# Optimization experiments

Hardware: AMD Instinct MI355X
Metric: run time of the kernel (lower is better)

The kernel has to match this reference:

```python
import jax, jax.numpy as jnp
import numpy as np

EPS = 1e-7  # K.epsilon()

_LC = np.zeros((3, 3, 3), np.float32)  # Levi-Civita for 1x1->1
_LC[0, 1, 2] = _LC[1, 2, 0] = _LC[2, 0, 1] = 1.0
_LC[0, 2, 1] = _LC[2, 1, 0] = _LC[1, 0, 2] = -1.0


def _ssp(x):
    # shifted softplus: log(0.5*exp(x)+0.5)
    return jnp.log(0.5 * jnp.exp(x) + 0.5)


def _radial(image, w1, b1, w2, b2):
    # Sequential([Dense(32), Dense(feat)]) -- linear Dense layers (no activation)
    return (image @ w1 + b1) @ w2 + b2  # (m, a, b, feat)


def setup_inputs() -> dict:
    key = jax.random.key(0)
    ks = jax.random.split(key, 16)
    M, A, RBF, F, SI, H = 4, 256, 64, 32, 32, 32
    inp = {}
    inp["image"] = jax.random.uniform(ks[0], (M, A, A, RBF), dtype=jnp.float32)
    inp["vectors"] = jax.random.normal(ks[1], (M, A, A, 3), dtype=jnp.float32)
    inp["feat0"] = jax.random.normal(ks[2], (M, A, F, 1), dtype=jnp.float32)
    inp["feat1"] = jax.random.normal(ks[3], (M, A, F, 3), dtype=jnp.float32)
    i = 4
    for rin in (0, 1):
        for fro in (0, 1):
            tag = f"{rin}{fro}"
            inp[f"w1_{tag}"] = jax.random.normal(ks[i], (RBF, H)) / np.sqrt(RBF).astype(np.float32)
            inp[f"b1_{tag}"] = jnp.zeros((H,), jnp.float32)
            i += 1
            inp[f"w2_{tag}"] = jax.random.normal(ks[i], (H, F)) / np.sqrt(np.float32(H))
            inp[f"b2_{tag}"] = jnp.zeros((F,), jnp.float32)
            i += 1
    inp["w_si0"] = jax.random.normal(ks[i], (SI, 2 * F)) / np.sqrt(np.float32(2 * F)); i += 1
    inp["w_si1"] = jax.random.normal(ks[i], (SI, 3 * F)) / np.sqrt(np.float32(3 * F)); i += 1
    inp["b_act0"] = jnp.zeros((SI,), jnp.float32)
    inp["b_act1"] = jnp.zeros((SI,), jnp.float32)
    return inp


def reference(image, vectors, feat0, feat1,
              w1_00, b1_00, w2_00, b2_00,
              w1_01, b1_01, w2_01, b2_01,
              w1_10, b1_10, w2_10, b2_10,
              w1_11, b1_11, w2_11, b2_11,
              w_si0, w_si1, b_act0, b_act1):
    # mask where |r_ab| < eps (self-pairs / padding)
    mask = (jnp.sqrt(jnp.sum(vectors * vectors, axis=-1)) < EPS)[..., None]  # (m,a,b,1)

    def filt0(w1, b1, w2, b2):
        return _radial(image, w1, b1, w2, b2)  # (m,a,b,F), implicit rep index of size 1

    def filt1(w1, b1, w2, b2):
        r = jnp.where(mask, 0.0, _radial(image, w1, b1, w2, b2))  # masked radial
        return vectors[:, :, :, None, :] * r[..., None]  # (m,a,b,F,3)

    f0_in0 = filt0(w1_00, b1_00, w2_00, b2_00)
    f1_in0 = filt1(w1_01, b1_01, w2_01, b2_01)
    f0_in1 = filt0(w1_10, b1_10, w2_10, b2_10)
    f1_in1 = filt1(w1_11, b1_11, w2_11, b2_11)

    # point convolution (sum over neighbor atoms b)
    out_0x0_0 = jnp.einsum('mabf,mbfj->mafj', f0_in0, feat0)   # (m,a,F,1)
    out_0x1_1 = jnp.einsum('mabfi,mbfj->mafi', f1_in0, feat0)  # (m,a,F,3)
    out_1x0_1 = jnp.einsum('mabf,mbfj->mafj', f0_in1, feat1)   # (m,a,F,3)
    cg0 = jnp.eye(3, dtype=image.dtype)[None]                  # (1,3,3): 1x1->0
    out_1x1_0 = jnp.einsum('ijk,mabfj,mbfk->mafi', cg0, f1_in1, feat1)  # (m,a,F,1)
    lc = jnp.asarray(_LC, image.dtype)                         # 1x1->1
    out_1x1_1 = jnp.einsum('ijk,mabfj,mbfk->mafi', lc, f1_in1, feat1)   # (m,a,F,3)

    # concat along channel dim per output RO
    cat0 = jnp.concatenate([out_0x0_0, out_1x1_0], axis=2)  # (m,a,2F,1)
    cat1 = jnp.concatenate([out_0x1_1, out_1x0_1, out_1x1_1], axis=2)  # (m,a,3F,3)

    # self-interaction: einsum('mafi,gf->maig') then transpose -> (m,a,g,i)
    si0 = jnp.einsum('mafi,gf->magi', cat0, w_si0)  # (m,a,SI,1)
    si1 = jnp.einsum('mafi,gf->magi', cat1, w_si1)  # (m,a,SI,3)

    # equivariant activation
    o0 = _ssp(si0 + b_act0[None, None, :, None])
    n1 = jnp.sqrt(jnp.maximum(jnp.sum(si1 * si1, axis=-1), EPS))  # norm_with_epsilon
    a1 = _ssp(n1 + b_act1)
    o1 = si1 * (a1 / n1)[..., None]
    return (o0, o1)
```

## Files before the change

### kernel.cpp

```cpp
#include <hip/hip_runtime.h>
#include <math.h>

#define M_ 4
#define A_ 256
#define RBF_ 64
#define F_ 32
#define H_ 32
#define SI_ 32
#define TF_ 128

typedef __attribute__((ext_vector_type(8))) short bf16x8;
typedef __attribute__((ext_vector_type(4))) float f32x4;
typedef __attribute__((ext_vector_type(3))) float f32x3;

__device__ __forceinline__ unsigned short f2bf(float f) {
  union { float f; unsigned u; } v; v.f = f;
  unsigned r = v.u + 0x7FFFu + ((v.u >> 16) & 1u);
  return (unsigned short)(r >> 16);
}

__device__ __forceinline__ unsigned pack2bf(float lo, float hi) {
  union { float f; unsigned u; } a, b; a.f = lo; b.f = hi;
  return __builtin_amdgcn_perm(b.u + 0x8000u, a.u + 0x8000u, 0x07060302u);
}

__device__ __forceinline__ float sspf(float x) {
  return fmaxf(x, 0.f) + log1pf(expf(-fabsf(x))) - 0.6931471805599453f;
}

__global__ __launch_bounds__(256) void combine_weights(
    const float* __restrict__ w1_00, const float* __restrict__ b1_00,
    const float* __restrict__ w2_00, const float* __restrict__ b2_00,
    const float* __restrict__ w1_01, const float* __restrict__ b1_01,
    const float* __restrict__ w2_01, const float* __restrict__ b2_01,
    const float* __restrict__ w1_10, const float* __restrict__ b1_10,
    const float* __restrict__ w2_10, const float* __restrict__ b2_10,
    const float* __restrict__ w1_11, const float* __restrict__ b1_11,
    const float* __restrict__ w2_11, const float* __restrict__ b2_11,
    unsigned short* __restrict__ wsT, float* __restrict__ bcw)
{
  const float* w1s[4] = {w1_00, w1_01, w1_10, w1_11};
  const float* b1s[4] = {b1_00, b1_01, b1_10, b1_11};
  const float* w2s[4] = {w2_00, w2_01, w2_10, w2_11};
  const float* b2s[4] = {b2_00, b2_01, b2_10, b2_11};
  int tid = blockIdx.x * 256 + threadIdx.x;
  int k   = tid >> 7;
  int tf  = tid & 127;
  int tag = tf >> 5, f = tf & 31;
  const float* w1 = w1s[tag];
  const float* w2 = w2s[tag];
  float s = 0.f;
  for (int h = 0; h < H_; ++h) s += w1[k * H_ + h] * w2[h * F_ + f];
  wsT[tf * 64 + k] = f2bf(s);
  if (tid < TF_) {
    const float* b1 = b1s[tag];
    const float* b2 = b2s[tag];
    float sb = b2[f];
    for (int h = 0; h < H_; ++h) sb += b1[h] * w2[h * F_ + f];
    bcw[tf] = sb;
  }
}

__global__ __launch_bounds__(512, 4) void conv_main(
    const float* __restrict__ image, const float* __restrict__ vectors,
    const float* __restrict__ feat0, const float* __restrict__ feat1,
    const unsigned short* __restrict__ wsT, const float* __restrict__ bcw,
    const float* __restrict__ w_si0, const float* __restrict__ w_si1,
    const float* __restrict__ b_act0, const float* __restrict__ b_act1,
    float* __restrict__ out)
{
  __shared__ __align__(16) char smem[39936];
  unsigned short* sA  = (unsigned short*)smem;
  float*          sV  = (float*)(smem + 36864);
  float*          cat = (float*)smem;

  const int t    = threadIdx.x;
  const int ma   = blockIdx.x;
  const int m    = ma >> 8;
  const int l    = t & 63;
  const int n    = l & 15;
  const int quad = l >> 4;
  const int wu    = __builtin_amdgcn_readfirstlane(t >> 6);
  const int which = wu & 1;
  const int tag   = wu >> 1;
  const int ct    = tag * 2 + which;
  const int f     = which * 16 + n;

  const unsigned short* wr = wsT + (ct * 16 + n) * 64 + quad * 8;
  const bf16x8 w0 = *(const bf16x8*)(wr);
  const bf16x8 w1 = *(const bf16x8*)(wr + 32);
  const float  bc = bcw[ct * 16 + n];

  const float* imgMA = image + (size_t)ma * A_ * RBF_;
  #pragma unroll
  for (int i = 0; i < 4; ++i) {
    int g = t + 512 * i;
    int r = g >> 3, c8 = g & 7;
    const float* src = imgMA + r * RBF_ + c8 * 8;
    float4 v0 = *(const float4*)(src);
    float4 v1 = *(const float4*)(src + 4);
    uint4 pk;
    pk.x = pack2bf(v0.x, v0.y);
    pk.y = pack2bf(v0.z, v0.w);
    pk.z = pack2bf(v1.x, v1.y);
    pk.w = pack2bf(v1.z, v1.w);
    *(uint4*)&sA[r * 72 + c8 * 8] = pk;
  }
  #pragma unroll
  for (int i = 0; i < 2; ++i) {
    int s = t + 512 * i;
    if (s < 768) sV[s] = vectors[(size_t)ma * (A_ * 3) + s];
  }

  const float* p0 = feat0 + (size_t)(m * A_) * F_ + f;
  const float* p1 = feat1 + ((size_t)(m * A_) * F_ + f) * 3;

  float gx[2][4], gy[2][4], gz[2][4];
  float pA = 0.f, pB0 = 0.f, pB1 = 0.f, pB2 = 0.f;

#define PF(BUF, BT) { \
    const int b0 = (BT) * 16 + quad * 4; \
    if (tag <= 1) { \
      _Pragma("unroll") \
      for (int r = 0; r < 4; ++r) gx[BUF][r] = p0[(b0 + r) * F_]; \
    } else { \
      _Pragma("unroll") \
      for (int r = 0; r < 4; ++r) { \
        f32x3 v = *(const f32x3*)&p1[(size_t)(b0 + r) * (F_ * 3)]; \
        gx[BUF][r] = v[0]; gy[BUF][r] = v[1]; gz[BUF][r] = v[2]; \
      } \
    } }

#define BODY(BT, BUF) { \
    const int brow = (BT) * 16; \
    const int lb   = brow + quad * 4; \
    const bf16x8 a0 = *(const bf16x8*)&sA[(brow + n) * 72 + quad * 8]; \
    const bf16x8 a1 = *(const bf16x8*)&sA[(brow + n) * 72 + 32 + quad * 8]; \
    f32x4 acc = {bc, bc, bc, bc}; \
    acc = __builtin_amdgcn_mfma_f32_16x16x32_bf16(a0, w0, acc, 0, 0, 0); \
    acc = __builtin_amdgcn_mfma_f32_16x16x32_bf16(a1, w1, acc, 0, 0, 0); \
    if (tag == 0) {             \
      _Pragma("unroll") \
      for (int r = 0; r < 4; ++r) pA += acc[r] * gx[BUF][r]; \
    } else if (tag == 1) {      \
      _Pragma("unroll") \
      for (int r = 0; r < 4; ++r) { \
        const float s  = acc[r] * gx[BUF][r]; \
        pB0 += sV[(lb + r) * 3 + 0] * s; \
        pB1 += sV[(lb + r) * 3 + 1] * s; \
        pB2 += sV[(lb + r) * 3 + 2] * s; \
      } \
    } else if (tag == 2) {      \
      _Pragma("unroll") \
      for (int r = 0; r < 4; ++r) { \
        const float Rr = acc[r]; \
        pB0 += Rr * gx[BUF][r]; pB1 += Rr * gy[BUF][r]; pB2 += Rr * gz[BUF][r]; \
      } \
    } else {                    \
      _Pragma("unroll") \
      for (int r = 0; r < 4; ++r) { \
        const float Rr = acc[r]; \
        const float ax = gx[BUF][r], ay = gy[BUF][r], az = gz[BUF][r]; \
        const float vx = sV[(lb + r) * 3 + 0]; \
        const float vy = sV[(lb + r) * 3 + 1]; \
        const float vz = sV[(lb + r) * 3 + 2]; \
        pA  += Rr * (vx * ax + vy * ay + vz * az); \
        pB0 += Rr * (vy * az - vz * ay); \
        pB1 += Rr * (vz * ax - vx * az); \
        pB2 += Rr * (vx * ay - vy * ax); \
      } \
    } }

  PF(0, 0)
  __syncthreads();

  #pragma unroll 1
  for (int bth = 0; bth < 8; ++bth) {
    const int bt0 = bth * 2;
    PF(1, bt0 + 1)
    BODY(bt0, 0)
    if (bth < 7) PF(0, bt0 + 2)
    BODY(bt0 + 1, 1)
  }

#define QRED(x) { x += __shfl_xor(x, 16); x += __shfl_xor(x, 32); }
  QRED(pA) QRED(pB0) QRED(pB1) QRED(pB2)

  __syncthreads();
  if (quad == 0) {
    if (tag == 0) {
      cat[f] = pA;
    } else if (tag == 1) {
      cat[64 + f * 3 + 0] = pB0;
      cat[64 + f * 3 + 1] = pB1;
      cat[64 + f * 3 + 2] = pB2;
    } else if (tag == 2) {
      cat[160 + f * 3 + 0] = pB0;
      cat[160 + f * 3 + 1] = pB1;
      cat[160 + f * 3 + 2] = pB2;
    } else {
      cat[32 + f] = pA;
      cat[256 + f * 3 + 0] = pB0;
      cat[256 + f * 3 + 1] = pB1;
      cat[256 + f * 3 + 2] = pB2;
    }
  }
  __syncthreads();

  const int outBase = ma * SI_;
  if (t < 32) {
    const float* wsr = w_si0 + t * 64;
    float s = 0.f;
    #pragma unroll 8
    for (int ff = 0; ff < 64; ++ff) s += cat[ff] * wsr[ff];
    s += b_act0[t];
    out[outBase + t] = sspf(s);
  } else if (t < 64) {
    int g = t - 32;
    const float* wsr = w_si1 + g * 96;
    float s0 = 0.f, s1 = 0.f, s2 = 0.f;
    #pragma unroll 8
    for (int ff = 0; ff < 96; ++ff) {
      float wv = wsr[ff];
      s0 += cat[64 + ff * 3 + 0] * wv;
      s1 += cat[64 + ff * 3 + 1] * wv;
      s2 += cat[64 + ff * 3 + 2] * wv;
    }
    float n2 = s0 * s0 + s1 * s1 + s2 * s2;
    float n1 = sqrtf(fmaxf(n2, 1e-7f));
    float a1 = sspf(n1 + b_act1[g]);
    float sc = a1 / n1;
    int ob = M_ * A_ * SI_ + (outBase + g) * 3;
    out[ob + 0] = s0 * sc;
    out[ob + 1] = s1 * sc;
    out[ob + 2] = s2 * sc;
  }
}

extern "C" void kernel_launch(void* const* d_in, const int* in_sizes, int n_in,
                              void* d_out, int out_size, void* d_ws, size_t ws_size,
                              hipStream_t stream) {
  const float* image   = (const float*)d_in[0];
  const float* vectors = (const float*)d_in[1];
  const float* feat0   = (const float*)d_in[2];
  const float* feat1   = (const float*)d_in[3];
  const float* w_si0   = (const float*)d_in[20];
  const float* w_si1   = (const float*)d_in[21];
  const float* b_act0  = (const float*)d_in[22];
  const float* b_act1  = (const float*)d_in[23];
  unsigned short* wsT = (unsigned short*)d_ws;
  float* bcw  = (float*)((char*)d_ws + 16384);
  float* out  = (float*)d_out;

  combine_weights<<<32, 256, 0, stream>>>(
      (const float*)d_in[4],  (const float*)d_in[5],
      (const float*)d_in[6],  (const float*)d_in[7],
      (const float*)d_in[8],  (const float*)d_in[9],
      (const float*)d_in[10], (const float*)d_in[11],
      (const float*)d_in[12], (const float*)d_in[13],
      (const float*)d_in[14], (const float*)d_in[15],
      (const float*)d_in[16], (const float*)d_in[17],
      (const float*)d_in[18], (const float*)d_in[19],
      wsT, bcw);

  conv_main<<<M_ * A_, 512, 0, stream>>>(
      image, vectors, feat0, feat1, wsT, bcw,
      w_si0, w_si1, b_act0, b_act1, out);
}
```

Before: 167.2 us.

## Split neighbor dimension across two blocks and move self-interaction to epilogue kernel

The main convolution kernel now processes half of the b-neighbors per block, doubling the grid to 2048 blocks and writing partial channel sums to workspace. A separate small kernel adds the two halves and performs the self-interaction and activation. The prefetch scheme changes to two independent register streams (rows 0-3 and 4-7 interleaved), and the shared-memory row stride changes to 158. This aims to improve occupancy, load balance and latency hiding, at the cost of an extra launch and a global round-trip for the partial sums.

```diff
diff --git a/kernel.cpp b/kernel.cpp
--- a/kernel.cpp
+++ b/kernel.cpp
@@ -8,6 +8,7 @@
 #define H_ 32
 #define SI_ 32
 #define TF_ 128
+#define SASTRIDE 158
 
 typedef __attribute__((ext_vector_type(8))) short bf16x8;
 typedef __attribute__((ext_vector_type(4))) float f32x4;
@@ -61,21 +62,19 @@
   }
 }
 
-__global__ __launch_bounds__(512, 4) void conv_main(
+__global__ __launch_bounds__(512, 4) void conv_partial(
     const float* __restrict__ image, const float* __restrict__ vectors,
     const float* __restrict__ feat0, const float* __restrict__ feat1,
     const unsigned short* __restrict__ wsT, const float* __restrict__ bcw,
-    const float* __restrict__ w_si0, const float* __restrict__ w_si1,
-    const float* __restrict__ b_act0, const float* __restrict__ b_act1,
-    float* __restrict__ out)
+    float* __restrict__ part)
 {
-  __shared__ __align__(16) char smem[39936];
-  unsigned short* sA  = (unsigned short*)smem;
-  float*          sV  = (float*)(smem + 36864);
-  float*          cat = (float*)smem;
+  __shared__ __align__(16) unsigned short sA[128 * SASTRIDE];
+  __shared__ float sV[128 * 3];
 
   const int t    = threadIdx.x;
-  const int ma   = blockIdx.x;
+  const int bid  = blockIdx.x;
+  const int ma   = bid >> 1;
+  const int half = bid & 1;
   const int m    = ma >> 8;
   const int l    = t & 63;
   const int n    = l & 15;
@@ -91,12 +90,12 @@
   const bf16x8 w1 = *(const bf16x8*)(wr + 32);
   const float  bc = bcw[ct * 16 + n];
 
-  const float* imgMA = image + (size_t)ma * A_ * RBF_;
+  const float* imgH = image + ((size_t)ma * A_ + half * 128) * RBF_;
   #pragma unroll
-  for (int i = 0; i < 4; ++i) {
+  for (int i = 0; i < 2; ++i) {
     int g = t + 512 * i;
     int r = g >> 3, c8 = g & 7;
-    const float* src = imgMA + r * RBF_ + c8 * 8;
+    const float* src = imgH + r * RBF_ + c8 * 8;
     float4 v0 = *(const float4*)(src);
     float4 v1 = *(const float4*)(src + 4);
     uint4 pk;
@@ -104,48 +103,45 @@
     pk.y = pack2bf(v0.z, v0.w);
     pk.z = pack2bf(v1.x, v1.y);
     pk.w = pack2bf(v1.z, v1.w);
-    *(uint4*)&sA[r * 72 + c8 * 8] = pk;
-  }
-  #pragma unroll
-  for (int i = 0; i < 2; ++i) {
-    int s = t + 512 * i;
-    if (s < 768) sV[s] = vectors[(size_t)ma * (A_ * 3) + s];
-  }
+    *(uint4*)&sA[r * SASTRIDE + c8 * 8] = pk;
+  }
+  if (t < 384) sV[t] = vectors[((size_t)ma * A_ + half * 128) * 3 + t];
 
   const float* p0 = feat0 + (size_t)(m * A_) * F_ + f;
   const float* p1 = feat1 + ((size_t)(m * A_) * F_ + f) * 3;
 
-  float gx[2][4], gy[2][4], gz[2][4];
+  float gxA[4], gyA[4], gzA[4];
+  float gxB[4], gyB[4], gzB[4];
   float pA = 0.f, pB0 = 0.f, pB1 = 0.f, pB2 = 0.f;
 
-#define PF(BUF, BT) { \
-    const int b0 = (BT) * 16 + quad * 4; \
+#define PF(GX, GY, GZ, BT) { \
+    const int b0 = half * 128 + (BT) * 16 + quad * 4; \
     if (tag <= 1) { \
       _Pragma("unroll") \
-      for (int r = 0; r < 4; ++r) gx[BUF][r] = p0[(b0 + r) * F_]; \
+      for (int r = 0; r < 4; ++r) GX[r] = p0[(b0 + r) * F_]; \
     } else { \
       _Pragma("unroll") \
       for (int r = 0; r < 4; ++r) { \
         f32x3 v = *(const f32x3*)&p1[(size_t)(b0 + r) * (F_ * 3)]; \
-        gx[BUF][r] = v[0]; gy[BUF][r] = v[1]; gz[BUF][r] = v[2]; \
+        GX[r] = v[0]; GY[r] = v[1]; GZ[r] = v[2]; \
       } \
     } }
 
-#define BODY(BT, BUF) { \
+#define BODY(BT, GX, GY, GZ) { \
     const int brow = (BT) * 16; \
     const int lb   = brow + quad * 4; \
-    const bf16x8 a0 = *(const bf16x8*)&sA[(brow + n) * 72 + quad * 8]; \
-    const bf16x8 a1 = *(const bf16x8*)&sA[(brow + n) * 72 + 32 + quad * 8]; \
+    const bf16x8 a0 = *(const bf16x8*)&sA[(brow + n) * SASTRIDE + quad * 8]; \
+    const bf16x8 a1 = *(const bf16x8*)&sA[(brow + n) * SASTRIDE + 32 + quad * 8]; \
     f32x4 acc = {bc, bc, bc, bc}; \
     acc = __builtin_amdgcn_mfma_f32_16x16x32_bf16(a0, w0, acc, 0, 0, 0); \
     acc = __builtin_amdgcn_mfma_f32_16x16x32_bf16(a1, w1, acc, 0, 0, 0); \
     if (tag == 0) {             \
       _Pragma("unroll") \
-      for (int r = 0; r < 4; ++r) pA += acc[r] * gx[BUF][r]; \
+      for (int r = 0; r < 4; ++r) pA += acc[r] * GX[r]; \
     } else if (tag == 1) {      \
       _Pragma("unroll") \
       for (int r = 0; r < 4; ++r) { \
-        const float s  = acc[r] * gx[BUF][r]; \
+        const float s  = acc[r] * GX[r]; \
         pB0 += sV[(lb + r) * 3 + 0] * s; \
         pB1 += sV[(lb + r) * 3 + 1] * s; \
         pB2 += sV[(lb + r) * 3 + 2] * s; \
@@ -154,13 +150,13 @@
       _Pragma("unroll") \
       for (int r = 0; r < 4; ++r) { \
         const float Rr = acc[r]; \
-        pB0 += Rr * gx[BUF][r]; pB1 += Rr * gy[BUF][r]; pB2 += Rr * gz[BUF][r]; \
+        pB0 += Rr * GX[r]; pB1 += Rr * GY[r]; pB2 += Rr * GZ[r]; \
       } \
     } else {                    \
       _Pragma("unroll") \
       for (int r = 0; r < 4; ++r) { \
         const float Rr = acc[r]; \
-        const float ax = gx[BUF][r], ay = gy[BUF][r], az = gz[BUF][r]; \
+        const float ax = GX[r], ay = GY[r], az = GZ[r]; \
         const float vx = sV[(lb + r) * 3 + 0]; \
         const float vy = sV[(lb + r) * 3 + 1]; \
         const float vz = sV[(lb + r) * 3 + 2]; \
@@ -171,57 +167,67 @@
       } \
     } }
 
-  PF(0, 0)
+  PF(gxA, gyA, gzA, 0)
+  PF(gxB, gyB, gzB, 4)
   __syncthreads();
 
   #pragma unroll 1
-  for (int bth = 0; bth < 8; ++bth) {
-    const int bt0 = bth * 2;
-    PF(1, bt0 + 1)
-    BODY(bt0, 0)
-    if (bth < 7) PF(0, bt0 + 2)
-    BODY(bt0 + 1, 1)
+  for (int it = 0; it < 4; ++it) {
+    BODY(it, gxA, gyA, gzA)
+    if (it < 3) PF(gxA, gyA, gzA, it + 1)
+    BODY(4 + it, gxB, gyB, gzB)
+    if (it < 3) PF(gxB, gyB, gzB, 4 + it + 1)
   }
 
 #define QRED(x) { x += __shfl_xor(x, 16); x += __shfl_xor(x, 32); }
   QRED(pA) QRED(pB0) QRED(pB1) QRED(pB2)
-
-  __syncthreads();
   if (quad == 0) {
+    float* dst = part + ((size_t)ma * 2 + half) * 352;
     if (tag == 0) {
-      cat[f] = pA;
+      dst[f] = pA;
     } else if (tag == 1) {
-      cat[64 + f * 3 + 0] = pB0;
-      cat[64 + f * 3 + 1] = pB1;
-      cat[64 + f * 3 + 2] = pB2;
+      f32x3 v = {pB0, pB1, pB2};
+      *(f32x3*)&dst[64 + f * 3] = v;
     } else if (tag == 2) {
-      cat[160 + f * 3 + 0] = pB0;
-      cat[160 + f * 3 + 1] = pB1;
-      cat[160 + f * 3 + 2] = pB2;
+      f32x3 v = {pB0, pB1, pB2};
+      *(f32x3*)&dst[160 + f * 3] = v;
     } else {
-      cat[32 + f] = pA;
-      cat[256 + f * 3 + 0] = pB0;
-      cat[256 + f * 3 + 1] = pB1;
-      cat[256 + f * 3 + 2] = pB2;
+      dst[32 + f] = pA;
+      f32x3 v = {pB0, pB1, pB2};
+      *(f32x3*)&dst[256 + f * 3] = v;
     }
   }
+}
+
+__global__ __launch_bounds__(64) void si_epilogue(
+    const float* __restrict__ part,
+    const float* __restrict__ w_si0, const float* __restrict__ w_si1,
+    const float* __restrict__ b_act0, const float* __restrict__ b_act1,
+    float* __restrict__ out)
+{
+  __shared__ float cat[352];
+  const int ma = blockIdx.x;
+  const int t  = threadIdx.x;
+  const float* pA = part + (size_t)ma * 704;
+  const float* pB = pA + 352;
+  for (int s = t; s < 352; s += 64) cat[s] = pA[s] + pB[s];
   __syncthreads();
 
   const int outBase = ma * SI_;
   if (t < 32) {
-    const float* wsr = w_si0 + t * 64;
+    const float* wr = w_si0 + t * 64;
     float s = 0.f;
     #pragma unroll 8
-    for (int ff = 0; ff < 64; ++ff) s += cat[ff] * wsr[ff];
+    for (int ff = 0; ff < 64; ++ff) s += cat[ff] * wr[ff];
     s += b_act0[t];
     out[outBase + t] = sspf(s);
-  } else if (t < 64) {
+  } else {
     int g = t - 32;
-    const float* wsr = w_si1 + g * 96;
+    const float* wr = w_si1 + g * 96;
     float s0 = 0.f, s1 = 0.f, s2 = 0.f;
     #pragma unroll 8
     for (int ff = 0; ff < 96; ++ff) {
-      float wv = wsr[ff];
+      float wv = wr[ff];
       s0 += cat[64 + ff * 3 + 0] * wv;
       s1 += cat[64 + ff * 3 + 1] * wv;
       s2 += cat[64 + ff * 3 + 2] * wv;
@@ -250,6 +256,7 @@
   const float* b_act1  = (const float*)d_in[23];
   unsigned short* wsT = (unsigned short*)d_ws;
   float* bcw  = (float*)((char*)d_ws + 16384);
+  float* part = (float*)((char*)d_ws + 32768);
   float* out  = (float*)d_out;
 
   combine_weights<<<32, 256, 0, stream>>>(
@@ -263,7 +270,9 @@
       (const float*)d_in[18], (const float*)d_in[19],
       wsT, bcw);
 
-  conv_main<<<M_ * A_, 512, 0, stream>>>(
-      image, vectors, feat0, feat1, wsT, bcw,
-      w_si0, w_si1, b_act0, b_act1, out);
-}
+  conv_partial<<<2 * M_ * A_, 512, 0, stream>>>(
+      image, vectors, feat0, feat1, wsT, bcw, part);
+
+  si_epilogue<<<M_ * A_, 64, 0, stream>>>(
+      part, w_si0, w_si1, b_act0, b_act1, out);
+}
```

Result: slower. 170.8 us (+2.1%).
